# Kernel tuning notes

Hardware: AMD Instinct MI355X
Metric: run time of the kernel (lower is better)

Reference implementation:

```python
import jax, jax.numpy as jnp
import numpy as np

DIM = 768
HEADS = 12
HIDDEN = 4 * DIM
B, D, H, W = 4, 8, 14, 14


def setup_inputs() -> dict:
    key = jax.random.key(0)
    ks = jax.random.split(key, 16)
    s = lambda k, shape, fan: jax.random.normal(k, shape, jnp.float32) * (1.0 / np.sqrt(fan))
    return {
        "x": jax.random.normal(ks[0], (B, DIM, D, H, W), jnp.float32),
        "pos_w": s(ks[1], (DIM, 1, 3, 3, 3), 27),   # depthwise conv3d weight (OIDHW, groups=DIM)
        "pos_b": jnp.zeros((DIM,), jnp.float32),
        "ln1_w": jnp.ones((DIM,), jnp.float32),
        "ln1_b": jnp.zeros((DIM,), jnp.float32),
        "qkv_w": s(ks[2], (3 * DIM, DIM), DIM),      # torch Linear layout [out,in], no bias
        "proj_w": s(ks[3], (DIM, DIM), DIM),
        "proj_b": jnp.zeros((DIM,), jnp.float32),
        "ln2_w": jnp.ones((DIM,), jnp.float32),
        "ln2_b": jnp.zeros((DIM,), jnp.float32),
        "fc1_w": s(ks[4], (HIDDEN, DIM), DIM),
        "fc1_b": jnp.zeros((HIDDEN,), jnp.float32),
        "fc2_w": s(ks[5], (DIM, HIDDEN), HIDDEN),
        "fc2_b": jnp.zeros((DIM,), jnp.float32),
    }


def _layernorm(x, w, b, eps=1e-5):
    mu = jnp.mean(x, axis=-1, keepdims=True)
    var = jnp.var(x, axis=-1, keepdims=True)
    return (x - mu) * jax.lax.rsqrt(var + eps) * w + b


def _forward(x, pos_w, pos_b, ln1_w, ln1_b, qkv_w, proj_w, proj_b,
             ln2_w, ln2_b, fc1_w, fc1_b, fc2_w, fc2_b):
    Bs, C, Ds, Hs, Ws = x.shape
    # depthwise 3x3x3 conv positional embedding + residual
    pe = jax.lax.conv_general_dilated(
        x, pos_w, window_strides=(1, 1, 1), padding=[(1, 1)] * 3,
        dimension_numbers=("NCDHW", "OIDHW", "NCDHW"), feature_group_count=C)
    x = x + pe + pos_b[None, :, None, None, None] * 0 + jnp.zeros((), x.dtype)
    x = x + 0.0  # keep simple
    x = x - pe + pe + pos_b[None, :, None, None, None]  # fold bias into conv output
    # flatten to tokens [B, N, C]
    t = x.reshape(Bs, C, -1).transpose(0, 2, 1)
    N = t.shape[1]
    # attention
    h = _layernorm(t, ln1_w, ln1_b)
    qkv = (h @ qkv_w.T).reshape(Bs, N, 3, HEADS, C // HEADS)
    q, k, v = [qkv[:, :, i].transpose(0, 2, 1, 3) for i in range(3)]  # [B,h,N,d]
    scale = (C // HEADS) ** -0.5
    attn = jax.nn.softmax(jnp.einsum("bhnd,bhmd->bhnm", q, k) * scale, axis=-1)
    o = jnp.einsum("bhnm,bhmd->bhnd", attn, v).transpose(0, 2, 1, 3).reshape(Bs, N, C)
    t = t + o @ proj_w.T + proj_b
    # MLP
    h = _layernorm(t, ln2_w, ln2_b)
    h = jax.nn.gelu(h @ fc1_w.T + fc1_b, approximate=False)
    t = t + h @ fc2_w.T + fc2_b
    return t.transpose(0, 2, 1).reshape(Bs, C, Ds, Hs, Ws)


def reference(x, pos_w, pos_b, ln1_w, ln1_b, qkv_w, proj_w, proj_b,
              ln2_w, ln2_b, fc1_w, fc1_b, fc2_w, fc2_b):
    return _forward(x, pos_w, pos_b, ln1_w, ln1_b, qkv_w, proj_w, proj_b,
                    ln2_w, ln2_b, fc1_w, fc1_b, fc2_w, fc2_b)
```

## Files before the change

kernel.cpp:

```cpp
#include <hip/hip_runtime.h>
#include <hip/hip_bf16.h>


using bf16 = __hip_bfloat16;
typedef __bf16 bf16x8 __attribute__((ext_vector_type(8)));
typedef float f32x4 __attribute__((ext_vector_type(4)));

#define NTOK 1568
#define CDIM 768
#define NH 12
#define HD 64
#define HID 3072
#define BN 6272
#define QSCALE 0.1803368801111244f
#define ESHIFT 17.312340490667562f

static __device__ __forceinline__ float bf2f(bf16 x) { return __bfloat162float(x); }
static __device__ __forceinline__ bf16 f2bf(float x) { return __float2bfloat16(x); }
static __device__ __forceinline__ unsigned short bfbits(float f) {
  bf16 h = __float2bfloat16(f);
  return *reinterpret_cast<unsigned short*>(&h);
}
static __device__ __forceinline__ float u16f(unsigned short u) {
  return __uint_as_float(((unsigned)u) << 16);
}
static __device__ __forceinline__ bool probe_bf16(const unsigned* p) {
  return ((*p) & 0xFFFFu) == 0x3F80u;
}

struct IngestArgs {
  const void* src[13];
  bf16* dst[13];
  int off[14];
};
__global__ __launch_bounds__(256) void ingest_all(IngestArgs a, const unsigned* __restrict__ probe) {
  bool isbf = probe_bf16(probe);
  int i = blockIdx.x * 256 + threadIdx.x;
  if (i >= a.off[13]) return;
  int j = 0;
  #pragma unroll
  for (int s = 0; s < 12; s++) if (i >= a.off[s + 1]) j = s + 1;
  int li = i - a.off[j];
  if (isbf) a.dst[j][li] = ((const bf16*)a.src[j])[li];
  else      a.dst[j][li] = f2bf(((const float*)a.src[j])[li]);
}

#define CXS 597
__global__ __launch_bounds__(256) void conv_pe_kernel(
    const void* __restrict__ x, const bf16* __restrict__ pw,
    const bf16* __restrict__ pb, float* __restrict__ t,
    const unsigned* __restrict__ probe) {
  int c0 = blockIdx.x * 16;
  int bd = blockIdx.y;
  int b = bd >> 3, d = bd & 7;
  bool isbf = probe_bf16(probe);
  __shared__ float xs[16 * CXS];
  int tid = threadIdx.x;

  for (int idx = tid; idx < 2352; idx += 256) {
    int ci = idx / 147;
    int rem = idx - ci * 147;
    int dd = rem / 49;
    int f4 = rem - dd * 49;
    int ds = d - 1 + dd;
    float4 v = make_float4(0.f, 0.f, 0.f, 0.f);
    if ((unsigned)ds < 8u) {
      size_t off = ((size_t)(b * CDIM + c0 + ci) * 8 + ds) * 196 + f4 * 4;
      if (isbf) {
        const bf16* xp = (const bf16*)x + off;
        v = make_float4(bf2f(xp[0]), bf2f(xp[1]), bf2f(xp[2]), bf2f(xp[3]));
      } else {
        v = *reinterpret_cast<const float4*>((const float*)x + off);
      }
    }
    float* dst = &xs[ci * CXS + dd * 196 + f4 * 4];
    dst[0] = v.x; dst[1] = v.y; dst[2] = v.z; dst[3] = v.w;
  }

  int ci = tid & 15;
  float wl[27];
  #pragma unroll
  for (int j = 0; j < 27; j++) wl[j] = bf2f(pw[(c0 + ci) * 27 + j]);
  float pbci = bf2f(pb[c0 + ci]);
  __syncthreads();

  const float* xc = &xs[ci * CXS];
  for (int n = (tid >> 4); n < 196; n += 16) {
    int hh = n / 14, ww = n - hh * 14;
    float acc = xc[196 + n] + pbci;
    #pragma unroll
    for (int kh = -1; kh <= 1; kh++) {
      int h2 = hh + kh;
      if ((unsigned)h2 >= 14u) continue;
      #pragma unroll
      for (int kw = -1; kw <= 1; kw++) {
        int w2 = ww + kw;
        if ((unsigned)w2 >= 14u) continue;
        int base = h2 * 14 + w2;
        int wj = (kh + 1) * 3 + (kw + 1);
        acc += wl[wj]      * xc[base];
        acc += wl[9 + wj]  * xc[196 + base];
        acc += wl[18 + wj] * xc[392 + base];
      }
    }
    t[((size_t)b * NTOK + d * 196 + n) * CDIM + c0 + ci] = acc;
  }
}

__global__ __launch_bounds__(256) void ln_kernel(
    const float* __restrict__ t, const bf16* __restrict__ w,
    const bf16* __restrict__ bia, bf16* __restrict__ h) {
  int tid = threadIdx.x, wid = tid >> 6, lane = tid & 63;
  int m = blockIdx.x * 4 + wid;
  const float4* row4 = reinterpret_cast<const float4*>(t + (size_t)m * CDIM);
  float4 v0 = row4[lane], v1 = row4[lane + 64], v2 = row4[lane + 128];
  float s = v0.x + v0.y + v0.z + v0.w + v1.x + v1.y + v1.z + v1.w + v2.x + v2.y + v2.z + v2.w;
  float q = v0.x*v0.x + v0.y*v0.y + v0.z*v0.z + v0.w*v0.w +
            v1.x*v1.x + v1.y*v1.y + v1.z*v1.z + v1.w*v1.w +
            v2.x*v2.x + v2.y*v2.y + v2.z*v2.z + v2.w*v2.w;
  #pragma unroll
  for (int off = 32; off > 0; off >>= 1) {
    s += __shfl_xor(s, off);
    q += __shfl_xor(q, off);
  }
  float mu = s * (1.f / CDIM);
  float var = q * (1.f / CDIM) - mu * mu;
  float rstd = rsqrtf(fmaxf(var, 0.f) + 1e-5f);
  const ushort4* w4 = reinterpret_cast<const ushort4*>(w);
  const ushort4* b4 = reinterpret_cast<const ushort4*>(bia);
  ushort4* h4 = reinterpret_cast<ushort4*>(h + (size_t)m * CDIM);
  #pragma unroll
  for (int j = 0; j < 3; j++) {
    float4 v = (j == 0) ? v0 : (j == 1) ? v1 : v2;
    ushort4 ww = w4[lane + 64 * j];
    ushort4 bb = b4[lane + 64 * j];
    ushort4 oo;
    oo.x = bfbits((v.x - mu) * rstd * u16f(ww.x) + u16f(bb.x));
    oo.y = bfbits((v.y - mu) * rstd * u16f(ww.y) + u16f(bb.y));
    oo.z = bfbits((v.z - mu) * rstd * u16f(ww.z) + u16f(bb.z));
    oo.w = bfbits((v.w - mu) * rstd * u16f(ww.w) + u16f(bb.w));
    h4[lane + 64 * j] = oo;
  }
}

#define LDA 40

template <int EPI, int NT>
__global__ __launch_bounds__(256) void gemm128(
    const bf16* __restrict__ A, const bf16* __restrict__ W,
    const bf16* __restrict__ bias, float* __restrict__ resid,
    bf16* __restrict__ oq, bf16* __restrict__ okk, bf16* __restrict__ ovt,
    bf16* __restrict__ obf, int K) {
  constexpr int NI = NT / 32;
  __shared__ __align__(16) bf16 As[128 * LDA];
  __shared__ __align__(16) bf16 Bs[NT * LDA];
  int tid = threadIdx.x;
  int w = tid >> 6, lane = tid & 63, quad = lane >> 4, l16 = lane & 15;
  int wr = w >> 1, wc = w & 1;
  int m0 = blockIdx.x * 128, n0 = blockIdx.y * NT;

  int r0 = tid >> 2;
  int c0 = (tid & 3) * 8;
  const bf16* gA0 = A + (size_t)(m0 + r0) * K + c0;
  const bf16* gA1 = A + (size_t)(m0 + 64 + r0) * K + c0;
  const bf16* gB0 = W + (size_t)(n0 + r0) * K + c0;
  const bf16* gB1 = W + (size_t)(n0 + 64 + r0) * K + c0;
  bf16* lA0 = As + r0 * LDA + c0;
  bf16* lA1 = As + (64 + r0) * LDA + c0;
  bf16* lB0 = Bs + r0 * LDA + c0;
  bf16* lB1 = Bs + (64 + r0) * LDA + c0;

  f32x4 acc[4][NI];
  #pragma unroll
  for (int mi = 0; mi < 4; mi++)
    #pragma unroll
    for (int ni = 0; ni < NI; ni++) acc[mi][ni] = (f32x4){0.f, 0.f, 0.f, 0.f};

  bf16x8 ra0 = *reinterpret_cast<const bf16x8*>(gA0);
  bf16x8 ra1 = *reinterpret_cast<const bf16x8*>(gA1);
  bf16x8 rb0 = *reinterpret_cast<const bf16x8*>(gB0);
  bf16x8 rb1;
  if (NT == 128) rb1 = *reinterpret_cast<const bf16x8*>(gB1);

  for (int k0 = 0; k0 < K; k0 += 32) {
    *reinterpret_cast<bf16x8*>(lA0) = ra0;
    *reinterpret_cast<bf16x8*>(lA1) = ra1;
    *reinterpret_cast<bf16x8*>(lB0) = rb0;
    if (NT == 128) *reinterpret_cast<bf16x8*>(lB1) = rb1;
    __syncthreads();
    if (k0 + 32 < K) {
      ra0 = *reinterpret_cast<const bf16x8*>(gA0 + k0 + 32);
      ra1 = *reinterpret_cast<const bf16x8*>(gA1 + k0 + 32);
      rb0 = *reinterpret_cast<const bf16x8*>(gB0 + k0 + 32);
      if (NT == 128) rb1 = *reinterpret_cast<const bf16x8*>(gB1 + k0 + 32);
    }
    bf16x8 af[4], bfr[NI];
    #pragma unroll
    for (int mi = 0; mi < 4; mi++)
      af[mi] = *reinterpret_cast<const bf16x8*>(As + (wr * 64 + mi * 16 + l16) * LDA + quad * 8);
    #pragma unroll
    for (int ni = 0; ni < NI; ni++)
      bfr[ni] = *reinterpret_cast<const bf16x8*>(Bs + (wc * (NT / 2) + ni * 16 + l16) * LDA + quad * 8);
    #pragma unroll
    for (int mi = 0; mi < 4; mi++)
      #pragma unroll
      for (int ni = 0; ni < NI; ni++)
        acc[mi][ni] = __builtin_amdgcn_mfma_f32_16x16x32_bf16(af[mi], bfr[ni], acc[mi][ni], 0, 0, 0);
    __syncthreads();
  }

  int mrow0 = m0 + wr * 64 + quad * 4;
  #pragma unroll
  for (int mi = 0; mi < 4; mi++) {
    #pragma unroll
    for (int ni = 0; ni < NI; ni++) {
      int col0 = n0 + wc * (NT / 2) + ni * 16;
      int col = col0 + l16;
      if (EPI == 0) {
        int i3 = col0 / CDIM;
        int rem = col0 % CDIM;
        int head = rem >> 6;
        int ddb = rem & 63;
        if (i3 == 2) {
          int m4 = mrow0 + mi * 16;
          int b = m4 / NTOK, n4 = m4 % NTOK;
          ushort4 pk;
          pk.x = bfbits(acc[mi][ni][0]);
          pk.y = bfbits(acc[mi][ni][1]);
          pk.z = bfbits(acc[mi][ni][2]);
          pk.w = bfbits(acc[mi][ni][3]);
          size_t idx = ((size_t)(b * NH + head) * HD + ddb + l16) * NTOK + n4;
          *reinterpret_cast<ushort4*>(ovt + idx) = pk;
        } else {
          bf16* dst = (i3 == 0) ? oq : okk;
          float scale = (i3 == 0) ? QSCALE : 1.0f;
          int dd = ddb + l16;
          #pragma unroll
          for (int reg = 0; reg < 4; reg++) {
            int m = mrow0 + mi * 16 + reg;
            int b = m / NTOK, n = m % NTOK;
            dst[((size_t)(b * NH + head) * NTOK + n) * HD + dd] = f2bf(acc[mi][ni][reg] * scale);
          }
        }
      } else if (EPI == 1) {
        float bb = bf2f(bias[col]);
        #pragma unroll
        for (int reg = 0; reg < 4; reg++) {
          int m = mrow0 + mi * 16 + reg;
          size_t idx = (size_t)m * CDIM + col;
          resid[idx] = resid[idx] + acc[mi][ni][reg] + bb;
        }
      } else if (EPI == 2) {
        float bb = bf2f(bias[col]);
        #pragma unroll
        for (int reg = 0; reg < 4; reg++) {
          int m = mrow0 + mi * 16 + reg;
          float xg = acc[mi][ni][reg] + bb;
          float ge = 0.5f * xg * (1.0f + erff(xg * 0.70710678118f));
          obf[(size_t)m * HID + col] = f2bf(ge);
        }
      } else {
        float bb = bf2f(bias[col]);
        #pragma unroll
        for (int reg = 0; reg < 4; reg++) {
          int m = mrow0 + mi * 16 + reg;
          size_t idx = (size_t)m * CDIM + col;
          obf[idx] = f2bf(resid[idx] + acc[mi][ni][reg] + bb);
        }
      }
    }
  }
}

#define LDS_S 84
__global__ __launch_bounds__(256) void attn_mfma(
    const bf16* __restrict__ q, const bf16* __restrict__ k,
    const bf16* __restrict__ vt, bf16* __restrict__ o) {
  __shared__ bf16 Ks[64 * LDS_S];
  __shared__ bf16 Vs[64 * LDS_S];
  __shared__ bf16 Ps[4][16 * LDS_S];
  int tid = threadIdx.x;
  int w = tid >> 6, lane = tid & 63, quad = lane >> 4, l16 = lane & 15;
  int qt = blockIdx.x;
  int bh = blockIdx.y;
  int b = bh / NH, head = bh % NH;
  const size_t kbase = (size_t)bh * NTOK * HD;

  int qr = qt * 64 + w * 16 + l16;
  int qrc = min(qr, NTOK - 1);
  bf16x8 aq0 = *reinterpret_cast<const bf16x8*>(q + kbase + (size_t)qrc * HD + quad * 8);
  bf16x8 aq1 = *reinterpret_cast<const bf16x8*>(q + kbase + (size_t)qrc * HD + 32 + quad * 8);

  f32x4 oacc[4];
  #pragma unroll
  for (int di = 0; di < 4; di++) oacc[di] = (f32x4){0.f, 0.f, 0.f, 0.f};
  float lrow[4] = {0.f, 0.f, 0.f, 0.f};

  int sr0 = tid >> 3;
  int sc0 = (tid & 7) * 8;
  const bf16* gK = k + kbase + (size_t)sr0 * HD + sc0;
  const bf16* gV = vt + ((size_t)bh * HD + sr0) * NTOK + sc0;
  bf16* pw = Ps[w];

  bf16x8 rk0 = *reinterpret_cast<const bf16x8*>(gK);
  bf16x8 rk1 = *reinterpret_cast<const bf16x8*>(gK + 32 * HD);
  bf16x8 rv0 = *reinterpret_cast<const bf16x8*>(gV);
  bf16x8 rv1 = *reinterpret_cast<const bf16x8*>(gV + 32 * (size_t)NTOK);

  for (int t = 0; t < 25; t++) {
    *reinterpret_cast<bf16x8*>(Ks + sr0 * LDS_S + sc0) = rk0;
    *reinterpret_cast<bf16x8*>(Ks + (sr0 + 32) * LDS_S + sc0) = rk1;
    *reinterpret_cast<bf16x8*>(Vs + sr0 * LDS_S + sc0) = rv0;
    *reinterpret_cast<bf16x8*>(Vs + (sr0 + 32) * LDS_S + sc0) = rv1;
    __syncthreads();
    if (t < 24) {
      int m1 = (t + 1) * 64;
      rk0 = *reinterpret_cast<const bf16x8*>(gK + (size_t)m1 * HD);
      rk1 = *reinterpret_cast<const bf16x8*>(gK + (size_t)(m1 + 32) * HD);
      rv0 = *reinterpret_cast<const bf16x8*>(gV + m1);
      rv1 = *reinterpret_cast<const bf16x8*>(gV + 32 * (size_t)NTOK + m1);
    }

    f32x4 s[4];
    #pragma unroll
    for (int ni = 0; ni < 4; ni++) {
      bf16x8 b0 = *reinterpret_cast<const bf16x8*>(Ks + (ni * 16 + l16) * LDS_S + quad * 8);
      bf16x8 b1 = *reinterpret_cast<const bf16x8*>(Ks + (ni * 16 + l16) * LDS_S + 32 + quad * 8);
      f32x4 z = (f32x4){0.f, 0.f, 0.f, 0.f};
      z = __builtin_amdgcn_mfma_f32_16x16x32_bf16(aq0, b0, z, 0, 0, 0);
      z = __builtin_amdgcn_mfma_f32_16x16x32_bf16(aq1, b1, z, 0, 0, 0);
      s[ni] = z;
    }
    if (t == 24) {
      s[2] = (f32x4){-1e30f, -1e30f, -1e30f, -1e30f};
      s[3] = (f32x4){-1e30f, -1e30f, -1e30f, -1e30f};
    }

    #pragma unroll
    for (int ni = 0; ni < 4; ni++)
      #pragma unroll
      for (int r = 0; r < 4; r++)
        s[ni][r] = exp2f(s[ni][r] - ESHIFT);
    #pragma unroll
    for (int r = 0; r < 4; r++)
      lrow[r] += s[0][r] + s[1][r] + s[2][r] + s[3][r];

    #pragma unroll
    for (int ni = 0; ni < 4; ni++)
      #pragma unroll
      for (int r = 0; r < 4; r++)
        pw[(quad * 4 + r) * LDS_S + ni * 16 + l16] = f2bf(s[ni][r]);
    bf16x8 ap0 = *reinterpret_cast<const bf16x8*>(pw + l16 * LDS_S + quad * 8);
    bf16x8 ap1 = *reinterpret_cast<const bf16x8*>(pw + l16 * LDS_S + 32 + quad * 8);

    #pragma unroll
    for (int di = 0; di < 4; di++) {
      bf16x8 bv0 = *reinterpret_cast<const bf16x8*>(Vs + (di * 16 + l16) * LDS_S + quad * 8);
      bf16x8 bv1 = *reinterpret_cast<const bf16x8*>(Vs + (di * 16 + l16) * LDS_S + 32 + quad * 8);
      oacc[di] = __builtin_amdgcn_mfma_f32_16x16x32_bf16(ap0, bv0, oacc[di], 0, 0, 0);
      oacc[di] = __builtin_amdgcn_mfma_f32_16x16x32_bf16(ap1, bv1, oacc[di], 0, 0, 0);
    }
    __syncthreads();
  }

  #pragma unroll
  for (int r = 0; r < 4; r++) {
    float t_ = lrow[r];
    t_ += __shfl_xor(t_, 1);
    t_ += __shfl_xor(t_, 2);
    t_ += __shfl_xor(t_, 4);
    t_ += __shfl_xor(t_, 8);
    lrow[r] = t_;
  }

  int orow0 = qt * 64 + w * 16 + quad * 4;
  #pragma unroll
  for (int r = 0; r < 4; r++) {
    int row = orow0 + r;
    if (row < NTOK) {
      float inv = 1.0f / lrow[r];
      size_t obase = ((size_t)b * NTOK + row) * CDIM + head * HD + l16;
      #pragma unroll
      for (int di = 0; di < 4; di++)
        o[obase + di * 16] = f2bf(oacc[di][r] * inv);
    }
  }
}

__global__ __launch_bounds__(256) void out_transpose(
    const bf16* __restrict__ t3, bf16* __restrict__ ob, float* __restrict__ of,
    const unsigned* __restrict__ probe) {
  bool isbf = probe_bf16(probe);
  __shared__ float tile[32][33];
  int c0 = blockIdx.x * 32;
  int n0 = blockIdx.y * 32;
  int b = blockIdx.z;
  int tx = threadIdx.x & 31;
  int ty = threadIdx.x >> 5;
  for (int yy = ty; yy < 32; yy += 8)
    tile[yy][tx] = bf2f(t3[((size_t)b * NTOK + n0 + yy) * CDIM + c0 + tx]);
  __syncthreads();
  for (int yy = ty; yy < 32; yy += 8) {
    size_t oi = ((size_t)b * CDIM + c0 + yy) * NTOK + n0 + tx;
    float vv = tile[tx][yy];
    if (isbf) ob[oi] = f2bf(vv);
    else      of[oi] = vv;
  }
}

extern "C" void kernel_launch(void* const* d_in, const int* in_sizes, int n_in,
                              void* d_out, int out_size, void* d_ws, size_t ws_size,
                              hipStream_t stream) {
  const unsigned* probe = (const unsigned*)d_in[3];

  char* ws = (char*)d_ws;
  size_t cur = 0;
  auto alloc = [&](size_t bytes) -> char* {
    char* p = ws + cur;
    cur = (cur + bytes + 511) & ~(size_t)511;
    return p;
  };

  bf16* canon[14];
  IngestArgs ia;
  int tot = 0;
  canon[0] = nullptr;
  for (int i = 1; i < 14; i++) {
    canon[i] = (bf16*)alloc((size_t)in_sizes[i] * 2);
    ia.src[i - 1] = d_in[i];
    ia.dst[i - 1] = canon[i];
    ia.off[i - 1] = tot;
    tot += in_sizes[i];
  }
  ia.off[13] = tot;

  float* t  = (float*)alloc((size_t)BN * CDIM * 4);
  bf16*  R1 = (bf16*)alloc((size_t)BN * CDIM * 2);
  bf16*  R2 = (bf16*)alloc((size_t)BN * HID * 2);
  bf16* q  = R2;
  bf16* kk = R2 + (size_t)BN * CDIM;
  bf16* vt = R2 + (size_t)2 * BN * CDIM;
  bf16* g  = R2;
  (void)ws_size;

  ingest_all<<<(tot + 255) / 256, 256, 0, stream>>>(ia, probe);
  const bf16 *pos_w = canon[1], *pos_b = canon[2],
             *ln1_w = canon[3], *ln1_b = canon[4], *qkv_w = canon[5],
             *proj_w = canon[6], *proj_b = canon[7], *ln2_w = canon[8],
             *ln2_b = canon[9], *fc1_w = canon[10], *fc1_b = canon[11],
             *fc2_w = canon[12], *fc2_b = canon[13];

  conv_pe_kernel<<<dim3(CDIM / 16, 32), 256, 0, stream>>>(d_in[0], pos_w, pos_b, t, probe);
  ln_kernel<<<BN / 4, 256, 0, stream>>>(t, ln1_w, ln1_b, R1);
  gemm128<0, 128><<<dim3(BN / 128, 2304 / 128), 256, 0, stream>>>(
      R1, qkv_w, nullptr, nullptr, q, kk, vt, nullptr, CDIM);
  attn_mfma<<<dim3(25, 4 * NH), 256, 0, stream>>>(q, kk, vt, R1);
  gemm128<1, 64><<<dim3(BN / 128, CDIM / 64), 256, 0, stream>>>(
      R1, proj_w, proj_b, t, nullptr, nullptr, nullptr, nullptr, CDIM);
  ln_kernel<<<BN / 4, 256, 0, stream>>>(t, ln2_w, ln2_b, R1);
  gemm128<2, 128><<<dim3(BN / 128, HID / 128), 256, 0, stream>>>(
      R1, fc1_w, fc1_b, nullptr, nullptr, nullptr, nullptr, g, CDIM);
  gemm128<3, 64><<<dim3(BN / 128, CDIM / 64), 256, 0, stream>>>(
      g, fc2_w, fc2_b, t, nullptr, nullptr, nullptr, R1, HID);
  out_transpose<<<dim3(CDIM / 32, NTOK / 32, 4), 256, 0, stream>>>(
      R1, (bf16*)d_out, (float*)d_out, probe);
}
```

Baseline: 469.0 us.

## Double GEMM k-tile depth and drop register prefetch in GEMM and attention

The GEMM now loads a 64-wide K slab per iteration (LDS stride 68) and issues two MFMA sub-steps per barrier pair, halving the number of loop iterations and syncs. Both the GEMM and attention kernels drop the register-staged prefetch of the next tile and load global memory straight into LDS between two barriers. The intent is to cut register pressure and barrier count, at the cost of no longer overlapping global loads with compute.

```diff
diff --git a/kernel.cpp b/kernel.cpp
--- a/kernel.cpp
+++ b/kernel.cpp
@@ -143,7 +143,7 @@
   }
 }
 
-#define LDA 40
+#define LDB 68
 
 template <int EPI, int NT>
 __global__ __launch_bounds__(256) void gemm128(
@@ -152,23 +152,23 @@
     bf16* __restrict__ oq, bf16* __restrict__ okk, bf16* __restrict__ ovt,
     bf16* __restrict__ obf, int K) {
   constexpr int NI = NT / 32;
-  __shared__ __align__(16) bf16 As[128 * LDA];
-  __shared__ __align__(16) bf16 Bs[NT * LDA];
+  __shared__ __align__(16) bf16 As[128 * LDB];
+  __shared__ __align__(16) bf16 Bs[NT * LDB];
   int tid = threadIdx.x;
   int w = tid >> 6, lane = tid & 63, quad = lane >> 4, l16 = lane & 15;
   int wr = w >> 1, wc = w & 1;
   int m0 = blockIdx.x * 128, n0 = blockIdx.y * NT;
 
   int r0 = tid >> 2;
-  int c0 = (tid & 3) * 8;
-  const bf16* gA0 = A + (size_t)(m0 + r0) * K + c0;
-  const bf16* gA1 = A + (size_t)(m0 + 64 + r0) * K + c0;
-  const bf16* gB0 = W + (size_t)(n0 + r0) * K + c0;
-  const bf16* gB1 = W + (size_t)(n0 + 64 + r0) * K + c0;
-  bf16* lA0 = As + r0 * LDA + c0;
-  bf16* lA1 = As + (64 + r0) * LDA + c0;
-  bf16* lB0 = Bs + r0 * LDA + c0;
-  bf16* lB1 = Bs + (64 + r0) * LDA + c0;
+  int c8 = (tid & 3) * 8;
+  const bf16* gA0 = A + (size_t)(m0 + r0) * K + c8;
+  const bf16* gA1 = A + (size_t)(m0 + 64 + r0) * K + c8;
+  const bf16* gB0 = W + (size_t)(n0 + r0) * K + c8;
+  const bf16* gB1 = W + (size_t)(n0 + 64 + r0) * K + c8;
+  bf16* lA0 = As + r0 * LDB + c8;
+  bf16* lA1 = As + (64 + r0) * LDB + c8;
+  bf16* lB0 = Bs + r0 * LDB + c8;
+  bf16* lB1 = Bs + (64 + r0) * LDB + c8;
 
   f32x4 acc[4][NI];
   #pragma unroll
@@ -176,37 +176,36 @@
     #pragma unroll
     for (int ni = 0; ni < NI; ni++) acc[mi][ni] = (f32x4){0.f, 0.f, 0.f, 0.f};
 
-  bf16x8 ra0 = *reinterpret_cast<const bf16x8*>(gA0);
-  bf16x8 ra1 = *reinterpret_cast<const bf16x8*>(gA1);
-  bf16x8 rb0 = *reinterpret_cast<const bf16x8*>(gB0);
-  bf16x8 rb1;
-  if (NT == 128) rb1 = *reinterpret_cast<const bf16x8*>(gB1);
-
-  for (int k0 = 0; k0 < K; k0 += 32) {
-    *reinterpret_cast<bf16x8*>(lA0) = ra0;
-    *reinterpret_cast<bf16x8*>(lA1) = ra1;
-    *reinterpret_cast<bf16x8*>(lB0) = rb0;
-    if (NT == 128) *reinterpret_cast<bf16x8*>(lB1) = rb1;
+  for (int k0 = 0; k0 < K; k0 += 64) {
     __syncthreads();
-    if (k0 + 32 < K) {
-      ra0 = *reinterpret_cast<const bf16x8*>(gA0 + k0 + 32);
-      ra1 = *reinterpret_cast<const bf16x8*>(gA1 + k0 + 32);
-      rb0 = *reinterpret_cast<const bf16x8*>(gB0 + k0 + 32);
-      if (NT == 128) rb1 = *reinterpret_cast<const bf16x8*>(gB1 + k0 + 32);
-    }
-    bf16x8 af[4], bfr[NI];
-    #pragma unroll
-    for (int mi = 0; mi < 4; mi++)
-      af[mi] = *reinterpret_cast<const bf16x8*>(As + (wr * 64 + mi * 16 + l16) * LDA + quad * 8);
-    #pragma unroll
-    for (int ni = 0; ni < NI; ni++)
-      bfr[ni] = *reinterpret_cast<const bf16x8*>(Bs + (wc * (NT / 2) + ni * 16 + l16) * LDA + quad * 8);
-    #pragma unroll
-    for (int mi = 0; mi < 4; mi++)
+    *reinterpret_cast<bf16x8*>(lA0) = *reinterpret_cast<const bf16x8*>(gA0 + k0);
+    *reinterpret_cast<bf16x8*>(lA0 + 32) = *reinterpret_cast<const bf16x8*>(gA0 + k0 + 32);
+    *reinterpret_cast<bf16x8*>(lA1) = *reinterpret_cast<const bf16x8*>(gA1 + k0);
+    *reinterpret_cast<bf16x8*>(lA1 + 32) = *reinterpret_cast<const bf16x8*>(gA1 + k0 + 32);
+    *reinterpret_cast<bf16x8*>(lB0) = *reinterpret_cast<const bf16x8*>(gB0 + k0);
+    *reinterpret_cast<bf16x8*>(lB0 + 32) = *reinterpret_cast<const bf16x8*>(gB0 + k0 + 32);
+    if (NT == 128) {
+      *reinterpret_cast<bf16x8*>(lB1) = *reinterpret_cast<const bf16x8*>(gB1 + k0);
+      *reinterpret_cast<bf16x8*>(lB1 + 32) = *reinterpret_cast<const bf16x8*>(gB1 + k0 + 32);
+    }
+    __syncthreads();
+    #pragma unroll
+    for (int kk = 0; kk < 2; kk++) {
+      bf16x8 af[4], bfr[NI];
+      #pragma unroll
+      for (int mi = 0; mi < 4; mi++)
+        af[mi] = *reinterpret_cast<const bf16x8*>(
+            As + (wr * 64 + mi * 16 + l16) * LDB + kk * 32 + quad * 8);
       #pragma unroll
       for (int ni = 0; ni < NI; ni++)
-        acc[mi][ni] = __builtin_amdgcn_mfma_f32_16x16x32_bf16(af[mi], bfr[ni], acc[mi][ni], 0, 0, 0);
-    __syncthreads();
+        bfr[ni] = *reinterpret_cast<const bf16x8*>(
+            Bs + (wc * (NT / 2) + ni * 16 + l16) * LDB + kk * 32 + quad * 8);
+      #pragma unroll
+      for (int mi = 0; mi < 4; mi++)
+        #pragma unroll
+        for (int ni = 0; ni < NI; ni++)
+          acc[mi][ni] = __builtin_amdgcn_mfma_f32_16x16x32_bf16(af[mi], bfr[ni], acc[mi][ni], 0, 0, 0);
+    }
   }
 
   int mrow0 = m0 + wr * 64 + quad * 4;
@@ -276,9 +275,9 @@
 __global__ __launch_bounds__(256) void attn_mfma(
     const bf16* __restrict__ q, const bf16* __restrict__ k,
     const bf16* __restrict__ vt, bf16* __restrict__ o) {
-  __shared__ bf16 Ks[64 * LDS_S];
-  __shared__ bf16 Vs[64 * LDS_S];
-  __shared__ bf16 Ps[4][16 * LDS_S];
+  __shared__ __align__(16) bf16 Ks[64 * LDS_S];
+  __shared__ __align__(16) bf16 Vs[64 * LDS_S];
+  __shared__ __align__(16) bf16 Ps[4][16 * LDS_S];
   int tid = threadIdx.x;
   int w = tid >> 6, lane = tid & 63, quad = lane >> 4, l16 = lane & 15;
   int qt = blockIdx.x;
@@ -302,24 +301,18 @@
   const bf16* gV = vt + ((size_t)bh * HD + sr0) * NTOK + sc0;
   bf16* pw = Ps[w];
 
-  bf16x8 rk0 = *reinterpret_cast<const bf16x8*>(gK);
-  bf16x8 rk1 = *reinterpret_cast<const bf16x8*>(gK + 32 * HD);
-  bf16x8 rv0 = *reinterpret_cast<const bf16x8*>(gV);
-  bf16x8 rv1 = *reinterpret_cast<const bf16x8*>(gV + 32 * (size_t)NTOK);
-
   for (int t = 0; t < 25; t++) {
-    *reinterpret_cast<bf16x8*>(Ks + sr0 * LDS_S + sc0) = rk0;
-    *reinterpret_cast<bf16x8*>(Ks + (sr0 + 32) * LDS_S + sc0) = rk1;
-    *reinterpret_cast<bf16x8*>(Vs + sr0 * LDS_S + sc0) = rv0;
-    *reinterpret_cast<bf16x8*>(Vs + (sr0 + 32) * LDS_S + sc0) = rv1;
+    int m0 = t * 64;
     __syncthreads();
-    if (t < 24) {
-      int m1 = (t + 1) * 64;
-      rk0 = *reinterpret_cast<const bf16x8*>(gK + (size_t)m1 * HD);
-      rk1 = *reinterpret_cast<const bf16x8*>(gK + (size_t)(m1 + 32) * HD);
-      rv0 = *reinterpret_cast<const bf16x8*>(gV + m1);
-      rv1 = *reinterpret_cast<const bf16x8*>(gV + 32 * (size_t)NTOK + m1);
-    }
+    *reinterpret_cast<bf16x8*>(Ks + sr0 * LDS_S + sc0) =
+        *reinterpret_cast<const bf16x8*>(gK + (size_t)m0 * HD);
+    *reinterpret_cast<bf16x8*>(Ks + (sr0 + 32) * LDS_S + sc0) =
+        *reinterpret_cast<const bf16x8*>(gK + (size_t)(m0 + 32) * HD);
+    *reinterpret_cast<bf16x8*>(Vs + sr0 * LDS_S + sc0) =
+        *reinterpret_cast<const bf16x8*>(gV + m0);
+    *reinterpret_cast<bf16x8*>(Vs + (sr0 + 32) * LDS_S + sc0) =
+        *reinterpret_cast<const bf16x8*>(gV + 32 * (size_t)NTOK + m0);
+    __syncthreads();
 
     f32x4 s[4];
     #pragma unroll
@@ -360,7 +353,6 @@
       oacc[di] = __builtin_amdgcn_mfma_f32_16x16x32_bf16(ap0, bv0, oacc[di], 0, 0, 0);
       oacc[di] = __builtin_amdgcn_mfma_f32_16x16x32_bf16(ap1, bv1, oacc[di], 0, 0, 0);
     }
-    __syncthreads();
   }
 
   #pragma unroll
```

After: 622.1 us. 1.33x slower.

## Double-buffer GEMM LDS tiles and drop register prefetch in attention

Applied to the files above, without the earlier changes.

The GEMM kernel now uses two LDS buffers for A and B. The next k-tile is written into the alternate buffer after the MFMAs, so each iteration needs one barrier instead of two. The attention kernel drops its register prefetch of K/V: it loads each tile directly from global memory into LDS between two barriers. The GEMM change is meant to cut barrier stalls at the cost of twice the LDS. The attention change lowers register pressure but exposes global-load latency each iteration.

```diff
diff --git a/kernel.cpp b/kernel.cpp
--- a/kernel.cpp
+++ b/kernel.cpp
@@ -152,8 +152,8 @@
     bf16* __restrict__ oq, bf16* __restrict__ okk, bf16* __restrict__ ovt,
     bf16* __restrict__ obf, int K) {
   constexpr int NI = NT / 32;
-  __shared__ __align__(16) bf16 As[128 * LDA];
-  __shared__ __align__(16) bf16 Bs[NT * LDA];
+  __shared__ __align__(16) bf16 As[2][128 * LDA];
+  __shared__ __align__(16) bf16 Bs[2][NT * LDA];
   int tid = threadIdx.x;
   int w = tid >> 6, lane = tid & 63, quad = lane >> 4, l16 = lane & 15;
   int wr = w >> 1, wc = w & 1;
@@ -165,10 +165,6 @@
   const bf16* gA1 = A + (size_t)(m0 + 64 + r0) * K + c0;
   const bf16* gB0 = W + (size_t)(n0 + r0) * K + c0;
   const bf16* gB1 = W + (size_t)(n0 + 64 + r0) * K + c0;
-  bf16* lA0 = As + r0 * LDA + c0;
-  bf16* lA1 = As + (64 + r0) * LDA + c0;
-  bf16* lB0 = Bs + r0 * LDA + c0;
-  bf16* lB1 = Bs + (64 + r0) * LDA + c0;
 
   f32x4 acc[4][NI];
   #pragma unroll
@@ -181,14 +177,16 @@
   bf16x8 rb0 = *reinterpret_cast<const bf16x8*>(gB0);
   bf16x8 rb1;
   if (NT == 128) rb1 = *reinterpret_cast<const bf16x8*>(gB1);
+  *reinterpret_cast<bf16x8*>(As[0] + r0 * LDA + c0) = ra0;
+  *reinterpret_cast<bf16x8*>(As[0] + (64 + r0) * LDA + c0) = ra1;
+  *reinterpret_cast<bf16x8*>(Bs[0] + r0 * LDA + c0) = rb0;
+  if (NT == 128) *reinterpret_cast<bf16x8*>(Bs[0] + (64 + r0) * LDA + c0) = rb1;
+  __syncthreads();
 
   for (int k0 = 0; k0 < K; k0 += 32) {
-    *reinterpret_cast<bf16x8*>(lA0) = ra0;
-    *reinterpret_cast<bf16x8*>(lA1) = ra1;
-    *reinterpret_cast<bf16x8*>(lB0) = rb0;
-    if (NT == 128) *reinterpret_cast<bf16x8*>(lB1) = rb1;
-    __syncthreads();
-    if (k0 + 32 < K) {
+    int cb = (k0 >> 5) & 1;
+    bool more = (k0 + 32 < K);
+    if (more) {
       ra0 = *reinterpret_cast<const bf16x8*>(gA0 + k0 + 32);
       ra1 = *reinterpret_cast<const bf16x8*>(gA1 + k0 + 32);
       rb0 = *reinterpret_cast<const bf16x8*>(gB0 + k0 + 32);
@@ -197,16 +195,22 @@
     bf16x8 af[4], bfr[NI];
     #pragma unroll
     for (int mi = 0; mi < 4; mi++)
-      af[mi] = *reinterpret_cast<const bf16x8*>(As + (wr * 64 + mi * 16 + l16) * LDA + quad * 8);
+      af[mi] = *reinterpret_cast<const bf16x8*>(As[cb] + (wr * 64 + mi * 16 + l16) * LDA + quad * 8);
     #pragma unroll
     for (int ni = 0; ni < NI; ni++)
-      bfr[ni] = *reinterpret_cast<const bf16x8*>(Bs + (wc * (NT / 2) + ni * 16 + l16) * LDA + quad * 8);
+      bfr[ni] = *reinterpret_cast<const bf16x8*>(Bs[cb] + (wc * (NT / 2) + ni * 16 + l16) * LDA + quad * 8);
     #pragma unroll
     for (int mi = 0; mi < 4; mi++)
       #pragma unroll
       for (int ni = 0; ni < NI; ni++)
         acc[mi][ni] = __builtin_amdgcn_mfma_f32_16x16x32_bf16(af[mi], bfr[ni], acc[mi][ni], 0, 0, 0);
-    __syncthreads();
+    if (more) {
+      *reinterpret_cast<bf16x8*>(As[cb ^ 1] + r0 * LDA + c0) = ra0;
+      *reinterpret_cast<bf16x8*>(As[cb ^ 1] + (64 + r0) * LDA + c0) = ra1;
+      *reinterpret_cast<bf16x8*>(Bs[cb ^ 1] + r0 * LDA + c0) = rb0;
+      if (NT == 128) *reinterpret_cast<bf16x8*>(Bs[cb ^ 1] + (64 + r0) * LDA + c0) = rb1;
+      __syncthreads();
+    }
   }
 
   int mrow0 = m0 + wr * 64 + quad * 4;
@@ -276,9 +280,9 @@
 __global__ __launch_bounds__(256) void attn_mfma(
     const bf16* __restrict__ q, const bf16* __restrict__ k,
     const bf16* __restrict__ vt, bf16* __restrict__ o) {
-  __shared__ bf16 Ks[64 * LDS_S];
-  __shared__ bf16 Vs[64 * LDS_S];
-  __shared__ bf16 Ps[4][16 * LDS_S];
+  __shared__ __align__(16) bf16 Ks[64 * LDS_S];
+  __shared__ __align__(16) bf16 Vs[64 * LDS_S];
+  __shared__ __align__(16) bf16 Ps[4][16 * LDS_S];
   int tid = threadIdx.x;
   int w = tid >> 6, lane = tid & 63, quad = lane >> 4, l16 = lane & 15;
   int qt = blockIdx.x;
@@ -302,24 +306,18 @@
   const bf16* gV = vt + ((size_t)bh * HD + sr0) * NTOK + sc0;
   bf16* pw = Ps[w];
 
-  bf16x8 rk0 = *reinterpret_cast<const bf16x8*>(gK);
-  bf16x8 rk1 = *reinterpret_cast<const bf16x8*>(gK + 32 * HD);
-  bf16x8 rv0 = *reinterpret_cast<const bf16x8*>(gV);
-  bf16x8 rv1 = *reinterpret_cast<const bf16x8*>(gV + 32 * (size_t)NTOK);
-
   for (int t = 0; t < 25; t++) {
-    *reinterpret_cast<bf16x8*>(Ks + sr0 * LDS_S + sc0) = rk0;
-    *reinterpret_cast<bf16x8*>(Ks + (sr0 + 32) * LDS_S + sc0) = rk1;
-    *reinterpret_cast<bf16x8*>(Vs + sr0 * LDS_S + sc0) = rv0;
-    *reinterpret_cast<bf16x8*>(Vs + (sr0 + 32) * LDS_S + sc0) = rv1;
+    int m0 = t * 64;
     __syncthreads();
-    if (t < 24) {
-      int m1 = (t + 1) * 64;
-      rk0 = *reinterpret_cast<const bf16x8*>(gK + (size_t)m1 * HD);
-      rk1 = *reinterpret_cast<const bf16x8*>(gK + (size_t)(m1 + 32) * HD);
-      rv0 = *reinterpret_cast<const bf16x8*>(gV + m1);
-      rv1 = *reinterpret_cast<const bf16x8*>(gV + 32 * (size_t)NTOK + m1);
-    }
+    *reinterpret_cast<bf16x8*>(Ks + sr0 * LDS_S + sc0) =
+        *reinterpret_cast<const bf16x8*>(gK + (size_t)m0 * HD);
+    *reinterpret_cast<bf16x8*>(Ks + (sr0 + 32) * LDS_S + sc0) =
+        *reinterpret_cast<const bf16x8*>(gK + (size_t)(m0 + 32) * HD);
+    *reinterpret_cast<bf16x8*>(Vs + sr0 * LDS_S + sc0) =
+        *reinterpret_cast<const bf16x8*>(gV + m0);
+    *reinterpret_cast<bf16x8*>(Vs + (sr0 + 32) * LDS_S + sc0) =
+        *reinterpret_cast<const bf16x8*>(gV + 32 * (size_t)NTOK + m0);
+    __syncthreads();
 
     f32x4 s[4];
     #pragma unroll
@@ -360,7 +358,6 @@
       oacc[di] = __builtin_amdgcn_mfma_f32_16x16x32_bf16(ap0, bv0, oacc[di], 0, 0, 0);
       oacc[di] = __builtin_amdgcn_mfma_f32_16x16x32_bf16(ap1, bv1, oacc[di], 0, 0, 0);
     }
-    __syncthreads();
   }
 
   #pragma unroll
```

After: 535.1 us. 14.1% more time.
